# Optimization experiments

Measured on AMD Instinct MI355X. Metric: run time of the kernel, lower is better.

Reference implementation:

```python
import jax, jax.numpy as jnp
import numpy as np

B = 32768   # batch
F = 32      # per-node feature dim
H = 256     # hidden width
M = 4       # modules per node
OUT = 8     # final output dim
INIT_W = 0.003
B_INIT = 0.1


def _lin(k, din, dout):
    # fanin_init-style uniform weights, bias filled with 0.1 (hidden layers)
    s = 1.0 / np.sqrt(din)
    W = jax.random.uniform(k, (M, din, dout), jnp.float32, -s, s)
    b = jnp.full((M, dout), B_INIT, jnp.float32)
    return W, b


def setup_inputs() -> dict:
    key = jax.random.key(0)
    ks = jax.random.split(key, 16)
    feats = jax.random.normal(ks[0], (B, 4 * F), jnp.float32)
    idx = jax.random.randint(ks[1], (B, 4), 0, M)
    onehots = jax.nn.one_hot(idx, M, dtype=jnp.float32).reshape(B, 4 * M)
    input_val = jnp.concatenate([feats, onehots], axis=1)  # [B,144]

    W00, b00 = _lin(ks[2], F, H)        # node0 post layer 0
    W01, b01 = _lin(ks[3], H, H)        # node0 post layer 1
    Wpre1, bpre1 = _lin(ks[4], F, H)    # node1 pre
    Wpost1, bpost1 = _lin(ks[5], 2 * H, H)  # node1 interface (prev 256 + own 256)
    Wpre2, bpre2 = _lin(ks[6], F, H)
    Wpost2, bpost2 = _lin(ks[7], 2 * H, H)
    Wpre3, bpre3 = _lin(ks[8], F, H)
    Wpost3, bpost3 = _lin(ks[9], 2 * H, H)
    # final output layer: uniform(-init_w, init_w) for W and b, identity act
    Wfin3 = jax.random.uniform(ks[10], (M, H, OUT), jnp.float32, -INIT_W, INIT_W)
    bfin3 = jax.random.uniform(ks[11], (M, OUT), jnp.float32, -INIT_W, INIT_W)
    return dict(input_val=input_val,
                W00=W00, b00=b00, W01=W01, b01=b01,
                Wpre1=Wpre1, bpre1=bpre1, Wpost1=Wpost1, bpost1=bpost1,
                Wpre2=Wpre2, bpre2=bpre2, Wpost2=Wpost2, bpost2=bpost2,
                Wpre3=Wpre3, bpre3=bpre3, Wpost3=Wpost3, bpost3=bpost3,
                Wfin3=Wfin3, bfin3=bfin3)


def _select(h, onehot):
    # per-row pick of the assigned module's output: [B,M,D],[B,M] -> [B,D]
    return jnp.einsum('bmo,bm->bo', h, onehot)


def reference(input_val, W00, b00, W01, b01,
              Wpre1, bpre1, Wpost1, bpost1,
              Wpre2, bpre2, Wpost2, bpost2,
              Wpre3, bpre3, Wpost3, bpost3,
              Wfin3, bfin3):
    feat = lambda j: input_val[:, j * F:(j + 1) * F]
    oh = lambda j: input_val[:, 4 * F + j * M: 4 * F + (j + 1) * M]

    # node 0: two hidden layers, module-dispatched (dense-all-modules + one-hot combine)
    h = jax.nn.relu(jnp.einsum('bi,mio->bmo', feat(0), W00) + b00)
    h = jax.nn.relu(jnp.einsum('bmi,mio->bmo', h, W01) + b01)
    x = _select(h, oh(0))  # [B,H]

    def node(x_prev, fj, ohj, Wpre, bpre, Wpost, bpost):
        hp = jax.nn.relu(jnp.einsum('bi,mio->bmo', fj, Wpre) + bpre)
        # interface layer consumes concat([x_prev, hp]); split the weight to
        # avoid materializing [B,M,2H]
        hq = jax.nn.relu(jnp.einsum('bi,mio->bmo', x_prev, Wpost[:, :H, :])
                         + jnp.einsum('bmi,mio->bmo', hp, Wpost[:, H:, :])
                         + bpost)
        return hq  # [B,M,H]

    x = _select(node(x, feat(1), oh(1), Wpre1, bpre1, Wpost1, bpost1), oh(1))
    x = _select(node(x, feat(2), oh(2), Wpre2, bpre2, Wpost2, bpost2), oh(2))

    h3 = node(x, feat(3), oh(3), Wpre3, bpre3, Wpost3, bpost3)  # [B,M,H]
    out = jnp.einsum('bmi,mio->bmo', h3, Wfin3) + bfin3          # final linear, identity act
    return _select(out, oh(3))  # [B,OUT]
```

## Files before the change

### kernel.cpp

```cpp
#include <hip/hip_runtime.h>

#define NB 32768
#define MAXTILE 768
#define ROWS 64
#define NT 4
#define XHS 536

typedef short s8v __attribute__((ext_vector_type(8)));
typedef short s4v __attribute__((ext_vector_type(4)));
typedef float f4v __attribute__((ext_vector_type(4)));
typedef unsigned short u16;
typedef unsigned short u16x4 __attribute__((ext_vector_type(4)));
typedef unsigned int u32;
typedef unsigned char u8;

__device__ __forceinline__ float bf2f(u16 u) { return __uint_as_float(((u32)u) << 16); }
__device__ __forceinline__ u16 f2bf(float f) {
    u32 x = __float_as_uint(f);
    x += 0x7FFFu + ((x >> 16) & 1u);
    return (u16)(x >> 16);
}
__device__ __forceinline__ s8v ld8(const u16* p) { return *reinterpret_cast<const s8v*>(p); }

#define MFMA16(a, b, c) __builtin_amdgcn_mfma_f32_16x16x32_bf16((a), (b), (c), 0, 0, 0)

template <int N> struct IC { static constexpr int v = N; };

__device__ __forceinline__ void detect_flag(const void* input, int tid, int* shflag)
{
    if (tid < 64) {
        u32 w = ((const u32*)input)[tid];
        u32 h0 = w & 0xFFFFu;
        u32 e0 = (h0 >> 7) & 0xFFu;
        bool plaus = (h0 == 0u) || (e0 >= 96u && e0 <= 143u);
        unsigned long long m = __ballot(plaus);
        if (tid == 0) *shflag = (__popcll(m) >= 48) ? 1 : 0;
    }
}

struct RepArgs {
    const void* W01; const void* Wp[3]; const void* pre[4]; const void* fin;
    const void* bias[9];
    u16 *rPre, *rW01, *rWp[3], *rFin, *cbias;
};

__global__ __launch_bounds__(256) void prepA_kernel(const void* __restrict__ inputv,
                                                    int* __restrict__ histT,
                                                    u16* __restrict__ keyloc,
                                                    RepArgs R)
{
    __shared__ int lcnt[256];
    __shared__ u16 T[2048];
    __shared__ int shmisc;
    int tid = threadIdx.x;
    int b = blockIdx.x;
    detect_flag(inputv, tid, &shmisc);
    __syncthreads();
    int flag = shmisc;

    if (b < 128) {
        lcnt[tid] = 0;
        __syncthreads();
        int row = (b << 8) + tid;
        const u32* in32 = (const u32*)inputv;
        const u16* in16 = (const u16*)inputv;
        int key = 0;
#pragma unroll
        for (int j = 0; j < 4; j++) {
            int base = row * 144 + 128 + j * 4;
            u32 v1, v2, v3;
            if (flag) { v1 = in16[base + 1]; v2 = in16[base + 2]; v3 = in16[base + 3]; }
            else      { v1 = in32[base + 1]; v2 = in32[base + 2]; v3 = in32[base + 3]; }
            int m = v1 ? 1 : (v2 ? 2 : (v3 ? 3 : 0));
            key |= m << (j << 1);
        }
        int loc = atomicAdd(&lcnt[key], 1);
        keyloc[row] = (u16)(key | (loc << 8));
        __syncthreads();
        histT[tid * 128 + b] = lcnt[tid];
        return;
    }

    int rb = b - 128;
    const void* src; u16* dst; int K, k0, mrow, kq;
    if (rb < 128) {
        int tile = rb >> 2; kq = rb & 3;
        int m = tile >> 3, s = tile & 7;
        src = R.W01; dst = R.rW01 + (m * 8 + s) * 8192; K = 256; k0 = s * 32; mrow = m;
    } else if (rb < 896) {
        int u = rb - 128, mat = u >> 8, r = u & 255;
        int tile = r >> 2; kq = r & 3;
        int m = tile >> 4, s = tile & 15;
        src = R.Wp[mat]; dst = R.rWp[mat] + (m * 16 + s) * 8192; K = 512; k0 = s * 32; mrow = m;
    } else if (rb < 960) {
        int u = rb - 896;
        int tile = u >> 2; kq = u & 3;
        int mat = tile >> 2, m = tile & 3;
        src = R.pre[mat]; dst = R.rPre + (mat * 4 + m) * 8192; K = 32; k0 = 0; mrow = m;
    } else if (rb < 964) {
        int m = rb - 960;
        const u16* s16 = (const u16*)R.fin;
        const float* s32 = (const float*)R.fin;
        u16* d = R.rFin + m * 4096;
        for (int half = 0; half < 2; half++) {
            for (int i = tid; i < 1024; i += 256) {
                int kk = half * 128 + (i >> 3);
                T[i] = flag ? s16[(m * 256 + kk) * 8 + (i & 7)]
                            : f2bf(s32[(m * 256 + kk) * 8 + (i & 7)]);
            }
            __syncthreads();
            for (int i = tid; i < 2048; i += 256) {
                int s = (half << 2) + (i >> 9), lane = (i >> 3) & 63, j = i & 7;
                int q = lane >> 4, l16 = lane & 15;
                int k = s * 32 + q * 8 + j;
                d[s * 512 + lane * 8 + j] = (l16 < 8) ? T[(k - half * 128) * 8 + l16] : (u16)0;
            }
            __syncthreads();
        }
        return;
    } else {
        const int sz[9] = {1024,1024,1024,1024,1024,1024,1024,1024,32};
        const int of[9] = {0,1024,2048,3072,4096,5120,6144,7168,8192};
        for (int i = tid; i < 8224; i += 256) {
            int t = i, e = 0;
            while (t >= sz[e]) { t -= sz[e]; e++; }
            R.cbias[of[e] + t] = flag ? ((const u16*)R.bias[e])[t]
                                      : f2bf(((const float*)R.bias[e])[t]);
        }
        return;
    }
    const u16* s16 = (const u16*)src;
    const float* s32 = (const float*)src;
    for (int i = tid; i < 2048; i += 256) {
        int kk = i >> 8, n = i & 255;
        int srcIdx = (mrow * K + k0 + kq * 8 + kk) * 256 + n;
        T[i] = flag ? s16[srcIdx] : f2bf(s32[srcIdx]);
    }
    __syncthreads();
    for (int i = tid; i < 2048; i += 256) {
        int mt = i >> 7, r = i & 127, l15 = r >> 3, j = i & 7;
        dst[mt * 512 + kq * 128 + r] = T[j * 256 + mt * 16 + l15];
    }
}

__global__ __launch_bounds__(256) void scatter_kernel(const int* __restrict__ histT,
                                                      const u16* __restrict__ keyloc,
                                                      int* __restrict__ perm,
                                                      int4* __restrict__ tileInfo,
                                                      int* __restrict__ tcount)
{
    __shared__ int lcnt[256];
    __shared__ int sBase[256];
    int tid = threadIdx.x;
    int b = blockIdx.x;

    const int4* hrow = (const int4*)(histT + tid * 128);
    int tot = 0, before = 0;
#pragma unroll
    for (int j = 0; j < 32; j++) {
        int4 h = hrow[j];
        int i4 = j << 2;
        tot += h.x + h.y + h.z + h.w;
        if (i4 + 0 < b) before += h.x;
        if (i4 + 1 < b) before += h.y;
        if (i4 + 2 < b) before += h.z;
        if (i4 + 3 < b) before += h.w;
    }
    lcnt[tid] = tot;
    __syncthreads();
    for (int off = 1; off < 256; off <<= 1) {
        int v = (tid >= off) ? lcnt[tid - off] : 0;
        __syncthreads();
        lcnt[tid] += v;
        __syncthreads();
    }
    int gbase = lcnt[tid] - tot;
    sBase[tid] = gbase + before;
    __syncthreads();

    if (b == 0) {
        int tiles = (tot + ROWS - 1) / ROWS;
        lcnt[tid] = tiles;
        __syncthreads();
        for (int off = 1; off < 256; off <<= 1) {
            int v = (tid >= off) ? lcnt[tid - off] : 0;
            __syncthreads();
            lcnt[tid] += v;
            __syncthreads();
        }
        int tbase = lcnt[tid] - tiles;
        int ttot = lcnt[255];
        if (tid == 0) tcount[0] = ttot;
        for (int t = 0; t < tiles; t++) {
            int rem = tot - t * ROWS;
            tileInfo[tbase + t] = make_int4(tid, gbase + t * ROWS, rem > ROWS ? ROWS : rem, 0);
        }
        for (int i = ttot + tid; i < MAXTILE; i += 256)
            tileInfo[i] = make_int4(0, 0, 0, 0);
    }

    int row = (b << 8) + tid;
    u32 kl = keyloc[row];
    int key = kl & 255, loc = kl >> 8;
    perm[sBase[key] + loc] = row;
}

struct MainP { const u16 *rPre, *rW01, *rWp1, *rWp2, *rWp3, *rFin, *cbias; };

__global__ __launch_bounds__(512, 4) void main_kernel(
    const void* __restrict__ inRaw,
    const int* __restrict__ perm, const int4* __restrict__ tileInfo,
    const int* __restrict__ tcount,
    MainP P, void* __restrict__ outp)
{
    __shared__ __align__(16) u16 xh[ROWS * XHS];
    __shared__ int rowids[ROWS];
    __shared__ int shflag;

    int tid = threadIdx.x;
    int lane = tid & 63, w = tid >> 6, quad = lane >> 4, l16 = lane & 15;

    int T = tcount[0];
    int tpx = (T + 7) >> 3;
    int x = blockIdx.x & 7, i = blockIdx.x >> 3;
    if (i >= tpx) return;
    int t = x * tpx + i;
    if (t >= T) return;
    int4 ti = tileInfo[t];
    int key = ti.x, ppos = ti.y, cntIn = ti.z;
    if (cntIn <= 0) return;

    detect_flag(inRaw, tid, &shflag);
    if (tid < ROWS) {
        int g = tid < cntIn ? tid : cntIn - 1;
        rowids[tid] = perm[ppos + g];
    }
    __syncthreads();
    int flag = shflag;
    int rows_[NT];
#pragma unroll
    for (int nt = 0; nt < NT; nt++) rows_[nt] = rowids[nt * 16 + l16];

    const u16* in16 = (const u16*)inRaw;
    const float* in32 = (const float*)inRaw;
    int mt0 = w << 1, mt1 = mt0 + 1;

    f4v acc0[NT], acc1[NT];

    auto gemm_run = [&](auto nc, const u16* Ab, int ks0) {
        constexpr int N = decltype(nc)::v;
        constexpr int D = 4;
        const u16* base0 = Ab + mt0 * 512 + lane * 8;
        const u16* base1 = Ab + mt1 * 512 + lane * 8;
        s8v A0[D], A1[D];
#pragma unroll
        for (int d = 0; d < D && d < N; d++) {
            A0[d] = ld8(base0 + d * 8192);
            A1[d] = ld8(base1 + d * 8192);
        }
        __syncthreads();
#pragma unroll
        for (int s = 0; s < N; s++) {
            s8v c0 = A0[s % D], c1 = A1[s % D];
            if (s + D < N) {
                A0[s % D] = ld8(base0 + (s + D) * 8192);
                A1[s % D] = ld8(base1 + (s + D) * 8192);
            }
#pragma unroll
            for (int nt = 0; nt < NT; nt++) {
                s8v B = ld8(&xh[(nt * 16 + l16) * XHS + (ks0 + s) * 32 + quad * 8]);
                acc0[nt] = MFMA16(c0, B, acc0[nt]);
                acc1[nt] = MFMA16(c1, B, acc1[nt]);
            }
        }
    };

    for (int node = 0; node < 4; node++) {
        int m = (key >> (node << 1)) & 3;

        s8v fb[NT];
#pragma unroll
        for (int nt = 0; nt < NT; nt++) {
            int off = rows_[nt] * 144 + (node << 5) + (quad << 3);
            if (flag) fb[nt] = ld8(in16 + off);
            else {
                f4v f0 = *(const f4v*)(in32 + off);
                f4v f1 = *(const f4v*)(in32 + off + 4);
                s8v r;
#pragma unroll
                for (int j = 0; j < 4; j++) { r[j] = (short)f2bf(f0[j]); r[4 + j] = (short)f2bf(f1[j]); }
                fb[nt] = r;
            }
        }

        const u16* preB = P.rPre + ((node << 2) + m) * 8192;
#pragma unroll
        for (int ci = 0; ci < 2; ci++) {
            int mt = mt0 + ci;
            s8v a = ld8(preB + mt * 512 + lane * 8);
            u16x4 bv = *(const u16x4*)(P.cbias + node * 2048 + m * 256 + mt * 16 + quad * 4);
            f4v bias;
#pragma unroll
            for (int r = 0; r < 4; r++) bias[r] = bf2f(bv[r]);
#pragma unroll
            for (int nt = 0; nt < NT; nt++) {
                f4v c = MFMA16(a, fb[nt], bias);
                s4v p;
#pragma unroll
                for (int r = 0; r < 4; r++) { float v = c[r] > 0.f ? c[r] : 0.f; p[r] = (short)f2bf(v); }
                *(s4v*)&xh[(nt * 16 + l16) * XHS + 256 + mt * 16 + quad * 4] = p;
            }
        }

        {
            u16x4 b0 = *(const u16x4*)(P.cbias + node * 2048 + 1024 + m * 256 + mt0 * 16 + quad * 4);
            u16x4 b1 = *(const u16x4*)(P.cbias + node * 2048 + 1024 + m * 256 + mt1 * 16 + quad * 4);
            f4v f0, f1;
#pragma unroll
            for (int r = 0; r < 4; r++) { f0[r] = bf2f(b0[r]); f1[r] = bf2f(b1[r]); }
#pragma unroll
            for (int nt = 0; nt < NT; nt++) { acc0[nt] = f0; acc1[nt] = f1; }
        }

        if (node == 0) gemm_run(IC<8>{},  P.rW01 + m * 8 * 8192, 8);
        else {
            const u16* WB = (node == 1 ? P.rWp1 : (node == 2 ? P.rWp2 : P.rWp3)) + m * 16 * 8192;
            gemm_run(IC<16>{}, WB, 0);
        }
        __syncthreads();

#pragma unroll
        for (int ci = 0; ci < 2; ci++) {
            int mt = mt0 + ci;
#pragma unroll
            for (int nt = 0; nt < NT; nt++) {
                f4v a = ci ? acc1[nt] : acc0[nt];
                s4v p;
#pragma unroll
                for (int r = 0; r < 4; r++) { float v = a[r] > 0.f ? a[r] : 0.f; p[r] = (short)f2bf(v); }
                *(s4v*)&xh[(nt * 16 + l16) * XHS + mt * 16 + quad * 4] = p;
            }
        }
    }
    __syncthreads();

    if (w < NT) {
        int m3 = (key >> 6) & 3;
        f4v c;
#pragma unroll
        for (int r = 0; r < 4; r++)
            c[r] = (quad < 2) ? bf2f(P.cbias[8192 + m3 * 8 + quad * 4 + r]) : 0.f;
#pragma unroll
        for (int s = 0; s < 8; s++) {
            s8v A = ld8(P.rFin + m3 * 4096 + s * 512 + lane * 8);
            s8v B = ld8(&xh[(w * 16 + l16) * XHS + s * 32 + quad * 8]);
            c = MFMA16(A, B, c);
        }
        int bidx = w * 16 + l16;
        if (quad < 2 && bidx < cntIn) {
            int row = rowids[bidx];
            if (flag) {
                s4v p;
#pragma unroll
                for (int r = 0; r < 4; r++) p[r] = (short)f2bf(c[r]);
                *(s4v*)((u16*)outp + row * 8 + quad * 4) = p;
            } else {
                *(f4v*)((float*)outp + row * 8 + quad * 4) = c;
            }
        }
    }
}

extern "C" void kernel_launch(void* const* d_in, const int* in_sizes, int n_in,
                              void* d_out, int out_size, void* d_ws, size_t ws_size,
                              hipStream_t stream)
{
    (void)in_sizes; (void)n_in; (void)out_size;
    const void* input  = d_in[0];
    const void* W00    = d_in[1];
    const void* b00    = d_in[2];
    const void* W01    = d_in[3];
    const void* b01    = d_in[4];
    const void* Wpre1  = d_in[5];
    const void* bpre1  = d_in[6];
    const void* Wpost1 = d_in[7];
    const void* bpost1 = d_in[8];
    const void* Wpre2  = d_in[9];
    const void* bpre2  = d_in[10];
    const void* Wpost2 = d_in[11];
    const void* bpost2 = d_in[12];
    const void* Wpre3  = d_in[13];
    const void* bpre3  = d_in[14];
    const void* Wpost3 = d_in[15];
    const void* bpost3 = d_in[16];
    const void* Wfin   = d_in[17];
    const void* bfin   = d_in[18];

    char* base = (char*)d_ws;
    size_t off = 0;
    auto alloc = [&](size_t bytes) -> char* {
        char* p = base + off;
        off += (bytes + 255) & ~(size_t)255;
        return p;
    };
    int*  histT     = (int*)alloc(256 * 128 * 4);
    u16*  keyloc    = (u16*)alloc(NB * 2);
    int4* tileInfo  = (int4*)alloc(MAXTILE * 16);
    int*  perm      = (int*)alloc((size_t)NB * 4);
    int*  tcount    = (int*)alloc(4);
    u16*  cbias    = (u16*)alloc(8224 * 2);
    u16*  rPre     = (u16*)alloc(131072 * 2);
    u16*  rW01     = (u16*)alloc(262144 * 2);
    u16*  rWp1     = (u16*)alloc(524288 * 2);
    u16*  rWp2     = (u16*)alloc(524288 * 2);
    u16*  rWp3     = (u16*)alloc(524288 * 2);
    u16*  rFin     = (u16*)alloc(16384 * 2);
    if (off > ws_size) return;

    RepArgs R;
    R.W01 = W01; R.Wp[0] = Wpost1; R.Wp[1] = Wpost2; R.Wp[2] = Wpost3;
    R.pre[0] = W00; R.pre[1] = Wpre1; R.pre[2] = Wpre2; R.pre[3] = Wpre3;
    R.fin = Wfin;
    R.bias[0] = b00;   R.bias[1] = b01;
    R.bias[2] = bpre1; R.bias[3] = bpost1;
    R.bias[4] = bpre2; R.bias[5] = bpost2;
    R.bias[6] = bpre3; R.bias[7] = bpost3;
    R.bias[8] = bfin;
    R.rPre = rPre; R.rW01 = rW01;
    R.rWp[0] = rWp1; R.rWp[1] = rWp2; R.rWp[2] = rWp3;
    R.rFin = rFin; R.cbias = cbias;

    prepA_kernel<<<1093, 256, 0, stream>>>(input, histT, keyloc, R);
    scatter_kernel<<<128, 256, 0, stream>>>(histT, keyloc, perm, tileInfo, tcount);

    MainP P;
    P.rPre = rPre; P.rW01 = rW01; P.rWp1 = rWp1; P.rWp2 = rWp2; P.rWp3 = rWp3;
    P.rFin = rFin; P.cbias = cbias;
    main_kernel<<<MAXTILE, 512, 0, stream>>>(input, perm, tileInfo, tcount, P, d_out);
}
```

Before: 194.7 us.

## Fuse scatter into prep kernel via flag-based inter-block sync; prefetch next features

Drops the separate scatter kernel. The 128 histogram blocks publish completion flags, a new coordinator block computes the global prefix sums and tile info, and the histogram blocks spin-wait on a release flag and then write the permutation themselves. This removes one kernel launch and the keyloc round trip. The main kernel also prefetches the next node's features during the current GEMM, and the weight pipeline depth goes from 4 to 6. The magic flags are never reset between calls, so later calls can read stale flags and race on histT and gbase. The spin-waits also assume the first 129 blocks are co-resident.

```diff
diff --git a/kernel.cpp b/kernel.cpp
--- a/kernel.cpp
+++ b/kernel.cpp
@@ -5,6 +5,8 @@
 #define ROWS 64
 #define NT 4
 #define XHS 536
+#define MAGIC1 0x13572468
+#define MAGIC2 0x2468ACE1
 
 typedef short s8v __attribute__((ext_vector_type(8)));
 typedef short s4v __attribute__((ext_vector_type(4)));
@@ -44,12 +46,18 @@
     u16 *rPre, *rW01, *rWp[3], *rFin, *cbias;
 };
 
-__global__ __launch_bounds__(256) void prepA_kernel(const void* __restrict__ inputv,
-                                                    int* __restrict__ histT,
-                                                    u16* __restrict__ keyloc,
-                                                    RepArgs R)
+__global__ __launch_bounds__(256) void prep_kernel(const void* __restrict__ inputv,
+                                                   int* __restrict__ histT,
+                                                   int* __restrict__ dflags,
+                                                   int* __restrict__ sflag,
+                                                   int* __restrict__ gbase,
+                                                   int* __restrict__ perm,
+                                                   int4* __restrict__ tileInfo,
+                                                   int* __restrict__ tcount,
+                                                   RepArgs R)
 {
     __shared__ int lcnt[256];
+    __shared__ int sBase[256];
     __shared__ u16 T[2048];
     __shared__ int shmisc;
     int tid = threadIdx.x;
@@ -57,6 +65,7 @@
     detect_flag(inputv, tid, &shmisc);
     __syncthreads();
     int flag = shmisc;
+    __syncthreads();
 
     if (b < 128) {
         lcnt[tid] = 0;
@@ -75,13 +84,83 @@
             key |= m << (j << 1);
         }
         int loc = atomicAdd(&lcnt[key], 1);
-        keyloc[row] = (u16)(key | (loc << 8));
         __syncthreads();
         histT[tid * 128 + b] = lcnt[tid];
+        __threadfence();
+        __syncthreads();
+        if (tid == 0)
+            __hip_atomic_store(&dflags[b], MAGIC1, __ATOMIC_RELEASE, __HIP_MEMORY_SCOPE_AGENT);
+        if (tid == 0) {
+            while (__hip_atomic_load(sflag, __ATOMIC_ACQUIRE, __HIP_MEMORY_SCOPE_AGENT) != MAGIC2)
+                __builtin_amdgcn_s_sleep(16);
+        }
+        __syncthreads();
+        __threadfence();
+        const int4* hrow = (const int4*)(histT + tid * 128);
+        int before = 0;
+#pragma unroll
+        for (int j = 0; j < 32; j++) {
+            int4 h = hrow[j];
+            int i4 = j << 2;
+            if (i4 + 0 < b) before += h.x;
+            if (i4 + 1 < b) before += h.y;
+            if (i4 + 2 < b) before += h.z;
+            if (i4 + 3 < b) before += h.w;
+        }
+        sBase[tid] = gbase[tid] + before;
+        __syncthreads();
+        perm[sBase[key] + loc] = row;
         return;
     }
 
-    int rb = b - 128;
+    if (b == 128) {
+        if (tid < 128) {
+            while (__hip_atomic_load(&dflags[tid], __ATOMIC_ACQUIRE, __HIP_MEMORY_SCOPE_AGENT) != MAGIC1)
+                __builtin_amdgcn_s_sleep(16);
+        }
+        __syncthreads();
+        __threadfence();
+        const int4* hrow = (const int4*)(histT + tid * 128);
+        int tot = 0;
+#pragma unroll
+        for (int j = 0; j < 32; j++) {
+            int4 h = hrow[j];
+            tot += h.x + h.y + h.z + h.w;
+        }
+        lcnt[tid] = tot;
+        __syncthreads();
+        for (int off = 1; off < 256; off <<= 1) {
+            int v = (tid >= off) ? lcnt[tid - off] : 0;
+            __syncthreads();
+            lcnt[tid] += v;
+            __syncthreads();
+        }
+        int gb = lcnt[tid] - tot;
+        gbase[tid] = gb;
+        int tiles = (tot + ROWS - 1) / ROWS;
+        __syncthreads();
+        lcnt[tid] = tiles;
+        __syncthreads();
+        for (int off = 1; off < 256; off <<= 1) {
+            int v = (tid >= off) ? lcnt[tid - off] : 0;
+            __syncthreads();
+            lcnt[tid] += v;
+            __syncthreads();
+        }
+        int tbase = lcnt[tid] - tiles;
+        if (tid == 255) tcount[0] = lcnt[255];
+        for (int t = 0; t < tiles; t++) {
+            int rem = tot - t * ROWS;
+            tileInfo[tbase + t] = make_int4(tid, gb + t * ROWS, rem > ROWS ? ROWS : rem, 0);
+        }
+        __threadfence();
+        __syncthreads();
+        if (tid == 0)
+            __hip_atomic_store(sflag, MAGIC2, __ATOMIC_RELEASE, __HIP_MEMORY_SCOPE_AGENT);
+        return;
+    }
+
+    int rb = b - 129;
     const void* src; u16* dst; int K, k0, mrow, kq;
     if (rb < 128) {
         int tile = rb >> 2; kq = rb & 3;
@@ -143,68 +222,6 @@
     }
 }
 
-__global__ __launch_bounds__(256) void scatter_kernel(const int* __restrict__ histT,
-                                                      const u16* __restrict__ keyloc,
-                                                      int* __restrict__ perm,
-                                                      int4* __restrict__ tileInfo,
-                                                      int* __restrict__ tcount)
-{
-    __shared__ int lcnt[256];
-    __shared__ int sBase[256];
-    int tid = threadIdx.x;
-    int b = blockIdx.x;
-
-    const int4* hrow = (const int4*)(histT + tid * 128);
-    int tot = 0, before = 0;
-#pragma unroll
-    for (int j = 0; j < 32; j++) {
-        int4 h = hrow[j];
-        int i4 = j << 2;
-        tot += h.x + h.y + h.z + h.w;
-        if (i4 + 0 < b) before += h.x;
-        if (i4 + 1 < b) before += h.y;
-        if (i4 + 2 < b) before += h.z;
-        if (i4 + 3 < b) before += h.w;
-    }
-    lcnt[tid] = tot;
-    __syncthreads();
-    for (int off = 1; off < 256; off <<= 1) {
-        int v = (tid >= off) ? lcnt[tid - off] : 0;
-        __syncthreads();
-        lcnt[tid] += v;
-        __syncthreads();
-    }
-    int gbase = lcnt[tid] - tot;
-    sBase[tid] = gbase + before;
-    __syncthreads();
-
-    if (b == 0) {
-        int tiles = (tot + ROWS - 1) / ROWS;
-        lcnt[tid] = tiles;
-        __syncthreads();
-        for (int off = 1; off < 256; off <<= 1) {
-            int v = (tid >= off) ? lcnt[tid - off] : 0;
-            __syncthreads();
-            lcnt[tid] += v;
-            __syncthreads();
-        }
-        int tbase = lcnt[tid] - tiles;
-        int ttot = lcnt[255];
-        if (tid == 0) tcount[0] = ttot;
-        for (int t = 0; t < tiles; t++) {
-            int rem = tot - t * ROWS;
-            tileInfo[tbase + t] = make_int4(tid, gbase + t * ROWS, rem > ROWS ? ROWS : rem, 0);
-        }
-        for (int i = ttot + tid; i < MAXTILE; i += 256)
-            tileInfo[i] = make_int4(0, 0, 0, 0);
-    }
-
-    int row = (b << 8) + tid;
-    u32 kl = keyloc[row];
-    int key = kl & 255, loc = kl >> 8;
-    perm[sBase[key] + loc] = row;
-}
-
 struct MainP { const u16 *rPre, *rW01, *rWp1, *rWp2, *rWp3, *rFin, *cbias; };
 
 __global__ __launch_bounds__(512, 4) void main_kernel(
@@ -246,10 +263,27 @@
     int mt0 = w << 1, mt1 = mt0 + 1;
 
     f4v acc0[NT], acc1[NT];
+    s8v fb[NT];
+
+    auto load_feats = [&](int node, s8v* dstv) {
+#pragma unroll
+        for (int nt = 0; nt < NT; nt++) {
+            int off = rows_[nt] * 144 + (node << 5) + (quad << 3);
+            if (flag) dstv[nt] = ld8(in16 + off);
+            else {
+                f4v f0 = *(const f4v*)(in32 + off);
+                f4v f1 = *(const f4v*)(in32 + off + 4);
+                s8v r;
+#pragma unroll
+                for (int j = 0; j < 4; j++) { r[j] = (short)f2bf(f0[j]); r[4 + j] = (short)f2bf(f1[j]); }
+                dstv[nt] = r;
+            }
+        }
+    };
 
     auto gemm_run = [&](auto nc, const u16* Ab, int ks0) {
         constexpr int N = decltype(nc)::v;
-        constexpr int D = 4;
+        constexpr int D = 6;
         const u16* base0 = Ab + mt0 * 512 + lane * 8;
         const u16* base1 = Ab + mt1 * 512 + lane * 8;
         s8v A0[D], A1[D];
@@ -275,23 +309,10 @@
         }
     };
 
+    load_feats(0, fb);
+
     for (int node = 0; node < 4; node++) {
         int m = (key >> (node << 1)) & 3;
-
-        s8v fb[NT];
-#pragma unroll
-        for (int nt = 0; nt < NT; nt++) {
-            int off = rows_[nt] * 144 + (node << 5) + (quad << 3);
-            if (flag) fb[nt] = ld8(in16 + off);
-            else {
-                f4v f0 = *(const f4v*)(in32 + off);
-                f4v f1 = *(const f4v*)(in32 + off + 4);
-                s8v r;
-#pragma unroll
-                for (int j = 0; j < 4; j++) { r[j] = (short)f2bf(f0[j]); r[4 + j] = (short)f2bf(f1[j]); }
-                fb[nt] = r;
-            }
-        }
 
         const u16* preB = P.rPre + ((node << 2) + m) * 8192;
 #pragma unroll
@@ -322,6 +343,9 @@
             for (int nt = 0; nt < NT; nt++) { acc0[nt] = f0; acc1[nt] = f1; }
         }
 
+        s8v fbn[NT];
+        if (node < 3) load_feats(node + 1, fbn);
+
         if (node == 0) gemm_run(IC<8>{},  P.rW01 + m * 8 * 8192, 8);
         else {
             const u16* WB = (node == 1 ? P.rWp1 : (node == 2 ? P.rWp2 : P.rWp3)) + m * 16 * 8192;
@@ -341,6 +365,8 @@
                 *(s4v*)&xh[(nt * 16 + l16) * XHS + mt * 16 + quad * 4] = p;
             }
         }
+#pragma unroll
+        for (int nt = 0; nt < NT; nt++) fb[nt] = fbn[nt];
     }
     __syncthreads();
 
@@ -404,7 +430,9 @@
         return p;
     };
     int*  histT     = (int*)alloc(256 * 128 * 4);
-    u16*  keyloc    = (u16*)alloc(NB * 2);
+    int*  dflags    = (int*)alloc(128 * 4);
+    int*  sflag     = (int*)alloc(4);
+    int*  gbase     = (int*)alloc(256 * 4);
     int4* tileInfo  = (int4*)alloc(MAXTILE * 16);
     int*  perm      = (int*)alloc((size_t)NB * 4);
     int*  tcount    = (int*)alloc(4);
@@ -430,8 +458,8 @@
     R.rWp[0] = rWp1; R.rWp[1] = rWp2; R.rWp[2] = rWp3;
     R.rFin = rFin; R.cbias = cbias;
 
-    prepA_kernel<<<1093, 256, 0, stream>>>(input, histT, keyloc, R);
-    scatter_kernel<<<128, 256, 0, stream>>>(histT, keyloc, perm, tileInfo, tcount);
+    prep_kernel<<<1094, 256, 0, stream>>>(input, histT, dflags, sflag, gbase,
+                                          perm, tileInfo, tcount, R);
 
     MainP P;
     P.rPre = rPre; P.rW01 = rW01; P.rWp1 = rWp1; P.rWp2 = rWp2; P.rWp3 = rWp3;
```

After: 244.4 us. 25.5% more time.
